# Performance work log

Measured on AMD Instinct MI355X. Metric: run time of the kernel, lower is better.

Reference implementation:

```python
import jax, jax.numpy as jnp
import numpy as np

PI = 3.1415927410125732
N = 4096
L = 1.28e-3          # box side [m]
VEL = 5e-7
RC = 3.15e-6         # Rc = diameter/2
RR = 8e-6
RO = 2.5e-5
RA = np.inf
DT_TRANS = 1.4e-14   # DT (translational diffusion)
DR = 0.0028
GAMMA = 25.0
DT = 0.2             # timestep dt
COLL_ITERS = 30      # fixed cap for collision-resolution do-while (orig caps at 1000)


def setup_inputs() -> dict:
    key = jax.random.key(0)
    ks = jax.random.split(key, 7)
    pos_re = jax.random.uniform(ks[0], (N,), jnp.float32) * L
    pos_im = jax.random.uniform(ks[1], (N,), jnp.float32) * L
    ang = jax.random.uniform(ks[2], (N,), jnp.float32, -PI, PI)
    ori_re = jnp.cos(ang)
    ori_im = jnp.sin(ang)
    deltas = jax.random.uniform(ks[3], (N,), jnp.float32) * 0.5
    rot_noise = jax.random.normal(ks[4], (N,), jnp.float32)
    tn_re = jax.random.normal(ks[5], (N,), jnp.float32)
    tn_im = jax.random.normal(ks[6], (N,), jnp.float32)
    return {"pos_re": pos_re, "pos_im": pos_im, "ori_re": ori_re, "ori_im": ori_im,
            "deltas": deltas, "rot_noise": rot_noise, "tn_re": tn_re, "tn_im": tn_im}


def _wrap(diff):
    # torch get_anglediff wrap: (-2pi,2pi) -> ~(-pi,pi)
    diff = jnp.where(diff <= -PI, jnp.mod(diff, PI), diff)
    return diff - (diff >= PI).astype(diff.dtype) * (2.0 * PI)


def _anglediff(a, b):
    return _wrap(jnp.angle(a) - jnp.angle(b))


def _cossim(a, b):
    # nn.CosineSimilarity(dim=1, eps=1e-14) on view_as_real vectors
    dot = a.real * b.real + a.imag * b.imag
    na = jnp.maximum(jnp.abs(a), 1e-14)
    nb = jnp.maximum(jnp.abs(b), 1e-14)
    return dot / (na * nb)


def _mvc(W, z):
    # real [n,n] mask @ complex [n] vector
    return W @ z.real + 1j * (W @ z.imag)


def _solve_collisions(pos):
    n = pos.shape[0]
    eye_f = jnp.eye(n, dtype=jnp.float32)
    eye_c = eye_f.astype(pos.dtype)

    def step(p):
        diff = p[None, :] - p[:, None] + eye_c  # [i,j] = pos_j - pos_i; diag dummy 1 (nan-safe)
        absd = jnp.abs(diff)
        coll = absd <= (2.0 * RC - eye_f)       # diag threshold negative -> self excluded
        move = jnp.where(coll, diff / jnp.where(coll, absd, 1.0) * ((2.1 * RC - absd) * 0.5), 0.0)
        return p - move.sum(axis=1), coll.sum()

    def body(carry, _):
        p, cont = carry
        p_new, ncoll = step(p)
        p = jnp.where(cont, p_new, p)           # do-while: apply move, then continue if collisions
        return (p, jnp.logical_and(cont, ncoll > 0)), None

    body = jax.checkpoint(body)
    (pos, _), _ = jax.lax.scan(body, (pos, jnp.array(True)), None, length=COLL_ITERS)
    return pos


def _forward(pos_re, pos_im, ori_re, ori_im, deltas, rot_noise, tn_re, tn_im):
    pos = (pos_re + 1j * pos_im).astype(jnp.complex64)
    ori = (ori_re + 1j * ori_im).astype(jnp.complex64)
    n = pos.shape[0]
    eye_b = jnp.eye(n, dtype=bool)

    # pairwise |pos_i - pos_j|; diag made 1 to keep abs() grad-safe (diag is masked out / re-added below)
    dists = jnp.abs(pos[:, None] - pos[None, :] + jnp.eye(n, dtype=pos.dtype))
    mask_rr = (dists <= RR) & ~eye_b              # repulsion zone, self excluded (eye subtracted in orig)
    mask_ro = (dists <= RO + RC) | eye_b          # orientation zone, self included (diag dist 0 in orig)
    mask_ra = (dists <= RA + RC) | eye_b          # Ra = inf -> all ones

    # alpha == 2*pi exactly -> within_view branch skipped (matches original)
    ang = jnp.angle(ori)
    abs_ad = jnp.abs(_wrap(ang[:, None] - ang[None, :]))
    in_front = abs_ad < PI / 2

    Wrr = (mask_rr & in_front).astype(jnp.float32)
    Wro = mask_ro.astype(jnp.float32)
    Wra = mask_ra.astype(jnp.float32)

    n_r = Wrr.sum(axis=1)
    S = _mvc(Wrr, pos) / jnp.maximum(n_r, 1.0) - pos * jnp.sign(n_r)
    d = -S

    n_a = Wra.sum(axis=1)
    cms = _mvc(Wra, pos) / jnp.maximum(n_a, 1.0)
    Ps = cms - pos * jnp.sign(n_a)

    osum = _mvc(Wro, ori)
    left = Ps * jnp.exp(1j * deltas)
    right = Ps * jnp.exp(-1j * deltas)

    # T (=300) >= T_release (=200): choose best turn by cosine similarity
    best = jnp.where(_cossim(left, osum) >= _cossim(right, osum), left, right)

    has_rep = jnp.abs(d) > 0.0
    d_safe = jnp.where(has_rep, d, jnp.ones_like(d))
    att = jnp.where(has_rep, _anglediff(d_safe, ori), _anglediff(best, ori))

    s2dr = np.float32(np.sqrt(2.0 * DR))
    sdt = np.float32(np.sqrt(DT))
    rot = jnp.exp(1j * (DT * GAMMA * DR * jnp.sin(att) + rot_noise * s2dr * sdt))

    # complex standard normal: real/imag each N(0, 1/sqrt(2))
    tnoise = (tn_re + 1j * tn_im) * np.float32(np.sqrt(0.5)) * np.float32(np.sqrt(2.0 * DT_TRANS))
    trans = DT * VEL * ori + tnoise * sdt

    new_pos = _solve_collisions(pos + trans)
    new_ori = ori * rot

    c2r = lambda z: jnp.stack([z.real, z.imag], axis=-1)
    # [5, N, 2]: positions, orientations, orientation_sums, leftturns, rightturns (real views)
    return jnp.stack([c2r(new_pos), c2r(new_ori), c2r(osum), c2r(left), c2r(right)], axis=0)


def reference(pos_re, pos_im, ori_re, ori_im, deltas, rot_noise, tn_re, tn_im):
    return _forward(pos_re, pos_im, ori_re, ori_im, deltas, rot_noise, tn_re, tn_im)
```

## Files before the change

### kernel.cpp

```cpp
#include <hip/hip_runtime.h>

#define NPART 4096
#define PI_F 3.1415927410125732f
#define TWO_PI_F 6.2831854820251465f
#define NBCAP 14336
#define SENT 4096

__device__ __forceinline__ float wrapf(float d) {
    if (d <= -PI_F) {
        d = fmodf(d, PI_F);
        if (d < 0.0f) d += PI_F;
    }
    if (d >= PI_F) d -= TWO_PI_F;
    return d;
}

__global__ __launch_bounds__(512)
void k_interact(const float* __restrict__ pr, const float* __restrict__ pim,
                const float* __restrict__ orr, const float* __restrict__ oim,
                const float* __restrict__ deltas,
                const float* __restrict__ rot_noise,
                const float* __restrict__ tn_re, const float* __restrict__ tn_im,
                float* __restrict__ out,
                float2* __restrict__ recPos, int* __restrict__ recMeta,
                unsigned short* __restrict__ recNbr, int* __restrict__ gcnt) {
    constexpr float RR_F  = 8e-6f;
    constexpr float RR2   = RR_F * RR_F;
    constexpr float ROC_F = (float)(2.5e-5 + 3.15e-6);
    constexpr float ROC2  = ROC_F * ROC_F;
    constexpr float CUT_F = 14.3e-6f;
    constexpr float CUT2  = CUT_F * CUT_F;

    __shared__ float4 ls4[512];
    __shared__ float red0[512], red1[512], red2[512], red3[512], red4[512];
    __shared__ float cr_[512], ci_[512];
    __shared__ int ncnt[8];
    __shared__ unsigned short nbrL[8 * 16];

    int tid = threadIdx.x;
    int li = tid & 7, sl = tid >> 3;
    int i = blockIdx.x * 8 + li;

    if (tid < 8) ncnt[tid] = 0;

    float px = pr[i], py = pim[i];
    float ox = orr[i], oy = oim[i];

    float n_r = 0.0f, S_re = 0.0f, S_im = 0.0f, o_re = 0.0f, o_im = 0.0f;
    float cs_re = 0.0f, cs_im = 0.0f;

    for (int c = 0; c < 8; ++c) {
        int j0 = c * 512;
        __syncthreads();
        float jr = pr[j0 + tid], ji = pim[j0 + tid];
        ls4[tid] = make_float4(jr, ji, orr[j0 + tid], oim[j0 + tid]);
        cs_re += jr; cs_im += ji;
        __syncthreads();
#pragma unroll
        for (int t = 0; t < 8; ++t) {
            int jj = sl * 8 + ((t + sl) & 7);
            int j = j0 + jj;
            float4 v = ls4[jj];
            float dr = px - v.x;
            float di = py - v.y;
            float d2 = dr * dr + di * di;
            if (__any(d2 <= ROC2)) {
                bool wro = d2 <= ROC2;
                float dot = ox * v.z + oy * v.w;
                bool wrr = (d2 <= RR2) & (dot > 0.0f) & (j != i);
                if (wro) { o_re += v.z; o_im += v.w; }
                if (wrr) { n_r += 1.0f; S_re += v.x; S_im += v.y; }
                if (d2 <= CUT2 && j != i) {
                    int slot = atomicAdd(&ncnt[li], 1);
                    if (slot < 16) nbrL[li * 16 + slot] = (unsigned short)j;
                }
            }
        }
    }

    red0[tid] = n_r; red1[tid] = S_re; red2[tid] = S_im;
    red3[tid] = o_re; red4[tid] = o_im;
    cr_[tid] = cs_re; ci_[tid] = cs_im;
    __syncthreads();
    for (int s = 256; s >= 8; s >>= 1) {
        if (tid < s) {
            red0[tid] += red0[tid + s]; red1[tid] += red1[tid + s];
            red2[tid] += red2[tid + s]; red3[tid] += red3[tid + s];
            red4[tid] += red4[tid + s];
            cr_[tid] += cr_[tid + s];  ci_[tid] += ci_[tid + s];
        }
        __syncthreads();
    }
    if (tid < 4) { cr_[tid] += cr_[tid + 4]; ci_[tid] += ci_[tid + 4]; }
    __syncthreads();
    if (tid < 2) { cr_[tid] += cr_[tid + 2]; ci_[tid] += ci_[tid + 2]; }
    __syncthreads();
    if (tid == 0) { cr_[0] += cr_[1]; ci_[0] += ci_[1]; }
    __syncthreads();

    if (tid < 8) {
        n_r = red0[tid]; S_re = red1[tid]; S_im = red2[tid];
        o_re = red3[tid]; o_im = red4[tid];

        float maxnr = fmaxf(n_r, 1.0f);
        float sgn = (n_r > 0.0f) ? 1.0f : 0.0f;
        float Sre = S_re / maxnr - px * sgn;
        float Sim = S_im / maxnr - py * sgn;
        float d_re = -Sre, d_im = -Sim;

        float cmsx = cr_[0] * (1.0f / 4096.0f);
        float cmsy = ci_[0] * (1.0f / 4096.0f);
        float Ps_re = cmsx - px;
        float Ps_im = cmsy - py;

        float dl = deltas[i];
        float cd = cosf(dl), sd = sinf(dl);
        float l_re = Ps_re * cd - Ps_im * sd;
        float l_im = Ps_re * sd + Ps_im * cd;
        float r_re = Ps_re * cd + Ps_im * sd;
        float r_im = Ps_im * cd - Ps_re * sd;

        float nb   = fmaxf(hypotf(o_re, o_im), 1e-14f);
        float na_l = fmaxf(hypotf(l_re, l_im), 1e-14f);
        float na_r = fmaxf(hypotf(r_re, r_im), 1e-14f);
        float csl = (l_re * o_re + l_im * o_im) / (na_l * nb);
        float csr = (r_re * o_re + r_im * o_im) / (na_r * nb);
        float b_re = (csl >= csr) ? l_re : r_re;
        float b_im = (csl >= csr) ? l_im : r_im;

        float ai = atan2f(oy, ox);
        bool has_rep = (d_re != 0.0f) || (d_im != 0.0f);
        float att;
        if (has_rep) att = wrapf(atan2f(d_im, d_re) - ai);
        else         att = wrapf(atan2f(b_im, b_re) - ai);

        constexpr float GDD  = (float)(0.2 * 25.0 * 0.0028);
        constexpr float S2DR = 0.07483314773547883f;
        constexpr float SDT  = 0.44721359549995793f;
        float theta = GDD * sinf(att) + (rot_noise[i] * S2DR) * SDT;
        float rr_ = cosf(theta), ri_ = sinf(theta);

        float no_re = ox * rr_ - oy * ri_;
        float no_im = ox * ri_ + oy * rr_;

        constexpr float DTVEL = (float)(0.2 * 5e-7);
        constexpr float C1 = 0.70710678118654752f;
        constexpr float C2 = 1.6733200530681511e-07f;
        float t_re = DTVEL * ox + ((tn_re[i] * C1) * C2) * SDT;
        float t_im = DTVEL * oy + ((tn_im[i] * C1) * C2) * SDT;
        float p0x = px + t_re, p0y = py + t_im;

        float2* o2 = (float2*)out;
        o2[i]            = make_float2(p0x, p0y);
        o2[1 * 4096 + i] = make_float2(no_re, no_im);
        o2[2 * 4096 + i] = make_float2(o_re, o_im);
        o2[3 * 4096 + i] = make_float2(l_re, l_im);
        o2[4 * 4096 + i] = make_float2(r_re, r_im);

        int c = min(ncnt[tid], 16);
        if (c > 0) {
            int cp = (c + 3) & ~3;
            int slot = atomicAdd(&gcnt[0], 1);
            int eoff = atomicAdd(&gcnt[1], cp);
            if (eoff + cp <= NBCAP) {
                recPos[slot] = make_float2(p0x, p0y);
                recMeta[slot] = i | (c << 12) | (eoff << 17);
                for (int m = 0; m < cp; ++m)
                    recNbr[eoff + m] = (m < c) ? nbrL[tid * 16 + m]
                                               : (unsigned short)SENT;
            } else {
                recPos[slot] = make_float2(p0x, p0y);
                recMeta[slot] = i;
            }
        }
    }
}

__global__ __launch_bounds__(512)
void k_coll_all(const float2* __restrict__ recPos, const int* __restrict__ recMeta,
                const unsigned short* __restrict__ recNbr,
                const int* __restrict__ gcnt, float* __restrict__ out) {
    constexpr float TWO_RC  = (float)(2.0 * 3.15e-6);
    constexpr float TWO_RC2 = TWO_RC * TWO_RC;
    constexpr float C21RC   = (float)(2.1 * 3.15e-6);

    __shared__ float2 pos[NPART + 2];
    __shared__ __align__(16) unsigned short nbr[NBCAP];
    __shared__ int flg[2];

    int tid = threadIdx.x;
    int n = gcnt[0];
    int totE = min(gcnt[1], NBCAP);

    int nU4 = (totE + 7) >> 3;
    const uint4* src4 = (const uint4*)recNbr;
    uint4* dst4 = (uint4*)nbr;
    for (int e = tid; e < nU4; e += 512) dst4[e] = src4[e];

    if (tid == 0) {
        pos[SENT] = make_float2(1e9f, 1e9f);
        flg[0] = 0; flg[1] = 0;
    }

    float myx[8], myy[8];
    int myi[8], myc[8], myo[8];
#pragma unroll
    for (int s = 0; s < 8; ++s) {
        int slot = s * 512 + tid;
        myc[s] = 0; myi[s] = SENT; myo[s] = 0;
        if (slot < n) {
            float2 p = recPos[slot];
            int meta = recMeta[slot];
            myx[s] = p.x; myy[s] = p.y;
            myi[s] = meta & 4095;
            myc[s] = (meta >> 12) & 31;
            myo[s] = (unsigned)meta >> 17;
            pos[myi[s]] = p;
        }
    }
    __syncthreads();

    int nq0[8], nq1[8], nq2[8], nq3[8];
#pragma unroll
    for (int s = 0; s < 8; ++s) {
        nq0[s] = SENT; nq1[s] = SENT; nq2[s] = SENT; nq3[s] = SENT;
        if (myc[s] > 0) {
            uint2 w = *(const uint2*)&nbr[myo[s]];
            nq0[s] = w.x & 0xffff; nq1[s] = w.x >> 16;
            nq2[s] = w.y & 0xffff; nq3[s] = w.y >> 16;
        }
    }

    for (int it = 0; it < 30; ++it) {
        float nx[8], ny[8];
        int ncs[8];
#pragma unroll
        for (int s = 0; s < 8; ++s) {
            ncs[s] = 0;
            int c = myc[s];
            if (c > 0) {
                float px = myx[s], py = myy[s];
                float mre = 0.0f, mim = 0.0f;
                int nc = 0;
                float2 q0 = pos[nq0[s]], q1 = pos[nq1[s]];
                float2 q2 = pos[nq2[s]], q3 = pos[nq3[s]];
#define COLL_ONE(q)                                                     \
                {                                                       \
                    float dr = (q).x - px, di = (q).y - py;             \
                    float d2 = dr * dr + di * di;                       \
                    if (d2 <= TWO_RC2) {                                \
                        float a = sqrtf(d2);                            \
                        float mm = (C21RC - a) * 0.5f / a;              \
                        mre += dr * mm; mim += di * mm; ++nc;           \
                    }                                                   \
                }
                COLL_ONE(q0) COLL_ONE(q1) COLL_ONE(q2) COLL_ONE(q3)
                for (int m0 = 4; m0 < c; m0 += 4) {
                    uint2 w = *(const uint2*)&nbr[myo[s] + m0];
                    int j0 = w.x & 0xffff, j1 = w.x >> 16;
                    int j2 = w.y & 0xffff, j3 = w.y >> 16;
                    float2 t0 = pos[j0], t1 = pos[j1], t2 = pos[j2], t3 = pos[j3];
                    COLL_ONE(t0) COLL_ONE(t1) COLL_ONE(t2) COLL_ONE(t3)
                }
#undef COLL_ONE
                ncs[s] = nc;
                nx[s] = px - mre; ny[s] = py - mim;
            }
        }
        __syncthreads();
#pragma unroll
        for (int s = 0; s < 8; ++s) {
            if (myc[s] > 0) {
                myx[s] = nx[s]; myy[s] = ny[s];
                pos[myi[s]] = make_float2(nx[s], ny[s]);
            }
        }
        int any = ncs[0] | ncs[1] | ncs[2] | ncs[3] |
                  ncs[4] | ncs[5] | ncs[6] | ncs[7];
        if (any) flg[it & 1] = 1;
        if (tid == 0) flg[(it + 1) & 1] = 0;
        __syncthreads();
        if (flg[it & 1] == 0) break;
    }

    float2* o2 = (float2*)out;
#pragma unroll
    for (int s = 0; s < 8; ++s)
        if (s * 512 + tid < n) o2[myi[s]] = make_float2(myx[s], myy[s]);
}

extern "C" void kernel_launch(void* const* d_in, const int* in_sizes, int n_in,
                              void* d_out, int out_size, void* d_ws, size_t ws_size,
                              hipStream_t stream) {
    const float* pos_re = (const float*)d_in[0];
    const float* pos_im = (const float*)d_in[1];
    const float* ori_re = (const float*)d_in[2];
    const float* ori_im = (const float*)d_in[3];
    const float* deltas = (const float*)d_in[4];
    const float* rot_noise = (const float*)d_in[5];
    const float* tn_re = (const float*)d_in[6];
    const float* tn_im = (const float*)d_in[7];
    float* out = (float*)d_out;

    int* gcnt = (int*)d_ws;
    float2* recPos = (float2*)((char*)d_ws + 16);
    int* recMeta   = (int*)(recPos + NPART);
    unsigned short* recNbr = (unsigned short*)(recMeta + NPART);

    hipMemsetAsync(gcnt, 0, 16, stream);
    k_interact<<<512, 512, 0, stream>>>(pos_re, pos_im, ori_re, ori_im,
                                        deltas, rot_noise, tn_re, tn_im,
                                        out, recPos, recMeta, recNbr, gcnt);
    k_coll_all<<<1, 512, 0, stream>>>(recPos, recMeta, recNbr, gcnt, out);
}
```

Measured before the change: 130.1 us.

## Process two particles per thread lane in interaction kernel to halve tile reloads

Each block of the interaction kernel now handles 16 target particles instead of 8, with each thread evaluating two targets against every staged neighbor. The grid shrinks to 256 blocks and the shared position/orientation tile is split so orientations are read only when a wave finds a neighbor in range. This halves how often the full particle array is streamed through shared memory per target, at the cost of more registers, more shared memory for duplicated reduction buffers and fewer blocks for occupancy. The collision kernel also changes its write-back condition from the neighbor count to the per-iteration collision flag, which affects which positions get updated.

```diff
diff --git a/kernel.cpp b/kernel.cpp
--- a/kernel.cpp
+++ b/kernel.cpp
@@ -31,62 +31,81 @@
     constexpr float CUT_F = 14.3e-6f;
     constexpr float CUT2  = CUT_F * CUT_F;
 
-    __shared__ float4 ls4[512];
-    __shared__ float red0[512], red1[512], red2[512], red3[512], red4[512];
+    __shared__ float2 lsP[512];
+    __shared__ float2 lsO[512];
+    __shared__ float rA0[512], rA1[512], rA2[512], rA3[512], rA4[512];
+    __shared__ float rB0[512], rB1[512], rB2[512], rB3[512], rB4[512];
     __shared__ float cr_[512], ci_[512];
-    __shared__ int ncnt[8];
-    __shared__ unsigned short nbrL[8 * 16];
+    __shared__ int ncnt[16];
+    __shared__ unsigned short nbrL[16 * 16];
 
     int tid = threadIdx.x;
     int li = tid & 7, sl = tid >> 3;
-    int i = blockIdx.x * 8 + li;
-
-    if (tid < 8) ncnt[tid] = 0;
-
-    float px = pr[i], py = pim[i];
-    float ox = orr[i], oy = oim[i];
-
-    float n_r = 0.0f, S_re = 0.0f, S_im = 0.0f, o_re = 0.0f, o_im = 0.0f;
+    int i0 = blockIdx.x * 16 + li;
+    int i1 = i0 + 8;
+
+    if (tid < 16) ncnt[tid] = 0;
+
+    float pxA = pr[i0], pyA = pim[i0], oxA = orr[i0], oyA = oim[i0];
+    float pxB = pr[i1], pyB = pim[i1], oxB = orr[i1], oyB = oim[i1];
+
+    float nAr = 0.0f, SAre = 0.0f, SAim = 0.0f, oAre = 0.0f, oAim = 0.0f;
+    float nBr = 0.0f, SBre = 0.0f, SBim = 0.0f, oBre = 0.0f, oBim = 0.0f;
     float cs_re = 0.0f, cs_im = 0.0f;
 
     for (int c = 0; c < 8; ++c) {
         int j0 = c * 512;
         __syncthreads();
         float jr = pr[j0 + tid], ji = pim[j0 + tid];
-        ls4[tid] = make_float4(jr, ji, orr[j0 + tid], oim[j0 + tid]);
+        lsP[tid] = make_float2(jr, ji);
+        lsO[tid] = make_float2(orr[j0 + tid], oim[j0 + tid]);
         cs_re += jr; cs_im += ji;
         __syncthreads();
 #pragma unroll
         for (int t = 0; t < 8; ++t) {
             int jj = sl * 8 + ((t + sl) & 7);
             int j = j0 + jj;
-            float4 v = ls4[jj];
-            float dr = px - v.x;
-            float di = py - v.y;
-            float d2 = dr * dr + di * di;
-            if (__any(d2 <= ROC2)) {
-                bool wro = d2 <= ROC2;
-                float dot = ox * v.z + oy * v.w;
-                bool wrr = (d2 <= RR2) & (dot > 0.0f) & (j != i);
-                if (wro) { o_re += v.z; o_im += v.w; }
-                if (wrr) { n_r += 1.0f; S_re += v.x; S_im += v.y; }
-                if (d2 <= CUT2 && j != i) {
+            float2 pv = lsP[jj];
+            float drA = pxA - pv.x, diA = pyA - pv.y;
+            float d2A = drA * drA + diA * diA;
+            float drB = pxB - pv.x, diB = pyB - pv.y;
+            float d2B = drB * drB + diB * diB;
+            if (__any((d2A <= ROC2) | (d2B <= ROC2))) {
+                float2 ov = lsO[jj];
+                if (d2A <= ROC2) { oAre += ov.x; oAim += ov.y; }
+                float dotA = oxA * ov.x + oyA * ov.y;
+                if ((d2A <= RR2) & (dotA > 0.0f) & (j != i0)) {
+                    nAr += 1.0f; SAre += pv.x; SAim += pv.y;
+                }
+                if (d2A <= CUT2 && j != i0) {
                     int slot = atomicAdd(&ncnt[li], 1);
                     if (slot < 16) nbrL[li * 16 + slot] = (unsigned short)j;
                 }
+                if (d2B <= ROC2) { oBre += ov.x; oBim += ov.y; }
+                float dotB = oxB * ov.x + oyB * ov.y;
+                if ((d2B <= RR2) & (dotB > 0.0f) & (j != i1)) {
+                    nBr += 1.0f; SBre += pv.x; SBim += pv.y;
+                }
+                if (d2B <= CUT2 && j != i1) {
+                    int slot = atomicAdd(&ncnt[li + 8], 1);
+                    if (slot < 16) nbrL[(li + 8) * 16 + slot] = (unsigned short)j;
+                }
             }
         }
     }
 
-    red0[tid] = n_r; red1[tid] = S_re; red2[tid] = S_im;
-    red3[tid] = o_re; red4[tid] = o_im;
+    rA0[tid] = nAr; rA1[tid] = SAre; rA2[tid] = SAim; rA3[tid] = oAre; rA4[tid] = oAim;
+    rB0[tid] = nBr; rB1[tid] = SBre; rB2[tid] = SBim; rB3[tid] = oBre; rB4[tid] = oBim;
     cr_[tid] = cs_re; ci_[tid] = cs_im;
     __syncthreads();
     for (int s = 256; s >= 8; s >>= 1) {
         if (tid < s) {
-            red0[tid] += red0[tid + s]; red1[tid] += red1[tid + s];
-            red2[tid] += red2[tid + s]; red3[tid] += red3[tid + s];
-            red4[tid] += red4[tid + s];
+            rA0[tid] += rA0[tid + s]; rA1[tid] += rA1[tid + s];
+            rA2[tid] += rA2[tid + s]; rA3[tid] += rA3[tid + s];
+            rA4[tid] += rA4[tid + s];
+            rB0[tid] += rB0[tid + s]; rB1[tid] += rB1[tid + s];
+            rB2[tid] += rB2[tid + s]; rB3[tid] += rB3[tid + s];
+            rB4[tid] += rB4[tid + s];
             cr_[tid] += cr_[tid + s];  ci_[tid] += ci_[tid + s];
         }
         __syncthreads();
@@ -98,9 +117,19 @@
     if (tid == 0) { cr_[0] += cr_[1]; ci_[0] += ci_[1]; }
     __syncthreads();
 
-    if (tid < 8) {
-        n_r = red0[tid]; S_re = red1[tid]; S_im = red2[tid];
-        o_re = red3[tid]; o_im = red4[tid];
+    if (tid < 16) {
+        int i = blockIdx.x * 16 + tid;
+        float n_r, S_re, S_im, o_re, o_im, px, py, ox, oy;
+        if (tid < 8) {
+            n_r = rA0[tid]; S_re = rA1[tid]; S_im = rA2[tid];
+            o_re = rA3[tid]; o_im = rA4[tid];
+            px = pxA; py = pyA; ox = oxA; oy = oyA;
+        } else {
+            int g = tid - 8;
+            n_r = rB0[g]; S_re = rB1[g]; S_im = rB2[g];
+            o_re = rB3[g]; o_im = rB4[g];
+            px = pxB; py = pyB; ox = oxB; oy = oyB;
+        }
 
         float maxnr = fmaxf(n_r, 1.0f);
         float sgn = (n_r > 0.0f) ? 1.0f : 0.0f;
@@ -270,7 +299,7 @@
         __syncthreads();
 #pragma unroll
         for (int s = 0; s < 8; ++s) {
-            if (myc[s] > 0) {
+            if (ncs[s] > 0) {
                 myx[s] = nx[s]; myy[s] = ny[s];
                 pos[myi[s]] = make_float2(nx[s], ny[s]);
             }
@@ -308,7 +337,7 @@
     unsigned short* recNbr = (unsigned short*)(recMeta + NPART);
 
     hipMemsetAsync(gcnt, 0, 16, stream);
-    k_interact<<<512, 512, 0, stream>>>(pos_re, pos_im, ori_re, ori_im,
+    k_interact<<<256, 512, 0, stream>>>(pos_re, pos_im, ori_re, ori_im,
                                         deltas, rot_noise, tn_re, tn_im,
                                         out, recPos, recMeta, recNbr, gcnt);
     k_coll_all<<<1, 512, 0, stream>>>(recPos, recMeta, recNbr, gcnt, out);
```

After: 129.7 us. Within noise of the previous version (-0.4%).
